# Kernel tuning notes

Measured on AMD Instinct MI355X. Metric: run time of the kernel, lower is better.

The kernel has to match this reference:

```python
import jax, jax.numpy as jnp
import numpy as np

D_MODEL = 1024
N_HEADS = 16
D_K = D_MODEL // N_HEADS  # 64, also d_v
B, S = 8, 1024


def setup_inputs() -> dict:
    key = jax.random.key(0)
    ks = jax.random.split(key, 12)
    sc = 1.0 / np.sqrt(D_MODEL)
    inp = {
        "q": jax.random.normal(ks[0], (B, S, D_MODEL), jnp.float32),
        "k": jax.random.normal(ks[1], (B, S, D_MODEL), jnp.float32),
        "v": jax.random.normal(ks[2], (B, S, D_MODEL), jnp.float32),
        # per-head projection weights stacked over heads; torch Linear stores [out,in]
        "Wq": jax.random.normal(ks[3], (N_HEADS, D_K, D_MODEL), jnp.float32) * sc,
        "bq": jax.random.normal(ks[4], (N_HEADS, D_K), jnp.float32) * sc,
        "Wk": jax.random.normal(ks[5], (N_HEADS, D_K, D_MODEL), jnp.float32) * sc,
        "bk": jax.random.normal(ks[6], (N_HEADS, D_K), jnp.float32) * sc,
        "Wv": jax.random.normal(ks[7], (N_HEADS, D_K, D_MODEL), jnp.float32) * sc,
        "bv": jax.random.normal(ks[8], (N_HEADS, D_K), jnp.float32) * sc,
        "Wf": jax.random.normal(ks[9], (D_MODEL, D_MODEL), jnp.float32) * sc,
        "bf": jax.random.normal(ks[10], (D_MODEL,), jnp.float32) * sc,
    }
    return inp


def reference(q, k, v, Wq, bq, Wk, bk, Wv, bv, Wf, bf):
    temper = jnp.asarray(D_K ** 0.5, q.dtype)
    # per-head linear projections, all heads at once: [b,s,h,dk]
    qh = jnp.einsum('bsd,hkd->bhsk', q, Wq) + bq[None, :, None, :]
    kh = jnp.einsum('bsd,hkd->bhsk', k, Wk) + bk[None, :, None, :]
    vh = jnp.einsum('bsd,hkd->bhsk', v, Wv) + bv[None, :, None, :]
    # scaled dot-product scores [b,h,s,s]
    scores = jnp.einsum('bhik,bhjk->bhij', qh, kh) / temper
    # faithful scalar-equality mask: positions exactly equal to mask (=0) -> -inf
    scores = jnp.where(scores == 0.0, -jnp.inf, scores)
    attn = jax.nn.softmax(scores, axis=-1)
    out = jnp.einsum('bhij,bhjv->bhiv', attn, vh)  # [b,h,s,dv]
    # concat heads (head order matches torch.cat over ModuleList)
    out = out.transpose(0, 2, 1, 3).reshape(out.shape[0], out.shape[2], -1)  # [b,s,d_model]
    return out @ Wf.T + bf
```

## Files before the change

### kernel.cpp

```cpp
#include <hip/hip_runtime.h>
#include <hip/hip_bf16.h>


#define D_MODEL_ 1024
#define NH_ 16
#define DK_ 64
#define B_ 8
#define S_ 1024
#define M_ (B_ * S_)

typedef __hip_bfloat16 bf16;
typedef __attribute__((ext_vector_type(8))) short short8;
typedef __attribute__((ext_vector_type(4))) short short4_t;
typedef __attribute__((ext_vector_type(4))) float f32x4;

typedef const __attribute__((address_space(1))) unsigned int* gas_u32p;
typedef __attribute__((address_space(3))) unsigned int* las_u32p;

__device__ __forceinline__ short f2bs(float x) {
  bf16 h = __float2bfloat16(x);
  return *reinterpret_cast<short*>(&h);
}

__global__ __launch_bounds__(256)
void conv_w4(const float* __restrict__ w0, const float* __restrict__ w1,
             const float* __restrict__ w2, const float* __restrict__ w3,
             bf16* __restrict__ out) {
  const float* src = (blockIdx.z == 0) ? w0 : (blockIdx.z == 1) ? w1
                   : (blockIdx.z == 2) ? w2 : w3;
  size_t i = ((size_t)blockIdx.x * 256 + threadIdx.x) * 8;
  f32x4 a = *(const f32x4*)(src + i);
  f32x4 b = *(const f32x4*)(src + i + 4);
  short8 s;
  s[0] = f2bs(a[0]); s[1] = f2bs(a[1]); s[2] = f2bs(a[2]); s[3] = f2bs(a[3]);
  s[4] = f2bs(b[0]); s[5] = f2bs(b[1]); s[6] = f2bs(b[2]); s[7] = f2bs(b[3]);
  *(short8*)((short*)out + (size_t)blockIdx.z * 1024 * 1024 + i) = s;
}

template<int BN, int AF32>
__device__ __forceinline__ void gemm_body(const void* __restrict__ A,
                                          const bf16* __restrict__ Wb,
                                          const float* __restrict__ bias,
                                          void* __restrict__ C,
                                          int cMode, float cscale, int m0, int n0)
{
  __shared__ short As[2][128 * 32];
  __shared__ short Bs[2][BN * 32];
  const int tid = threadIdx.x;
  const int lane = tid & 63;
  const int w = tid >> 6;
  const int l15 = lane & 15, quad = lane >> 4;
  const int wm = (w >> 1) * 64, wn = (w & 1) * (BN / 2);
  const int srow = lane >> 2;
  const int sslot = ((lane & 3) ^ ((lane >> 3) & 3)) * 8;
  const int rsl = (quad ^ ((l15 >> 1) & 3)) * 8;

  f32x4 au[4], av[4];
  auto loadAf = [&](int k0) {
    const float* Af = (const float*)A;
#pragma unroll
    for (int p = 0; p < 4; ++p) {
      int c = p * 256 + tid;
      int r = c >> 3, kc = (c & 7) * 8;
      const float* g = Af + (size_t)(m0 + r) * 1024 + k0 + kc;
      au[p] = *(const f32x4*)g;
      av[p] = *(const f32x4*)(g + 4);
    }
  };
  auto writeAf = [&]() {
#pragma unroll
    for (int p = 0; p < 4; ++p) {
      int c = p * 256 + tid;
      int r = c >> 3, kc = (c & 7) * 8;
      int s = (c & 3) ^ ((r >> 1) & 3);
      short8 sv;
      sv[0] = f2bs(au[p][0]); sv[1] = f2bs(au[p][1]); sv[2] = f2bs(au[p][2]); sv[3] = f2bs(au[p][3]);
      sv[4] = f2bs(av[p][0]); sv[5] = f2bs(av[p][1]); sv[6] = f2bs(av[p][2]); sv[7] = f2bs(av[p][3]);
      *(short8*)&As[kc >> 5][r * 32 + s * 8] = sv;
    }
  };

  f32x4 acc[4][BN / 32];
#pragma unroll
  for (int i = 0; i < 4; ++i)
#pragma unroll
    for (int j = 0; j < BN / 32; ++j)
      acc[i][j] = (f32x4){0.f, 0.f, 0.f, 0.f};

  if (AF32) loadAf(0);

  for (int k0 = 0; k0 < 1024; k0 += 64) {
    __syncthreads();
    if (AF32) {
      writeAf();
    } else {
      const bf16* Ab = (const bf16*)A;
#pragma unroll
      for (int sub = 0; sub < 2; ++sub)
#pragma unroll
        for (int p = 0; p < 2; ++p) {
          int r = 32 * w + 16 * p + srow;
          __builtin_amdgcn_global_load_lds(
              (gas_u32p)(const void*)(Ab + (size_t)(m0 + r) * 1024 + k0 + sub * 32 + sslot),
              (las_u32p)(void*)((char*)&As[sub][0] + w * 2048 + p * 1024), 16, 0, 0);
        }
    }
#pragma unroll
    for (int sub = 0; sub < 2; ++sub)
#pragma unroll
      for (int p = 0; p < BN / 64; ++p) {
        int r = (BN / 4) * w + 16 * p + srow;
        __builtin_amdgcn_global_load_lds(
            (gas_u32p)(const void*)(Wb + (size_t)(n0 + r) * 1024 + k0 + sub * 32 + sslot),
            (las_u32p)(void*)((char*)&Bs[sub][0] + w * (BN / 4) * 64 + p * 1024), 16, 0, 0);
      }
    __syncthreads();

    if (AF32 && k0 + 64 < 1024) loadAf(k0 + 64);

#pragma unroll
    for (int kk = 0; kk < 2; ++kk) {
      short8 af[4], bfv[BN / 32];
#pragma unroll
      for (int t = 0; t < 4; ++t)
        af[t]  = *(short8*)&As[kk][(wm + t * 16 + l15) * 32 + rsl];
#pragma unroll
      for (int t = 0; t < BN / 32; ++t)
        bfv[t] = *(short8*)&Bs[kk][(wn + t * 16 + l15) * 32 + rsl];
#pragma unroll
      for (int mt = 0; mt < 4; ++mt)
#pragma unroll
        for (int nt = 0; nt < BN / 32; ++nt)
          acc[mt][nt] = __builtin_amdgcn_mfma_f32_16x16x32_bf16(af[mt], bfv[nt], acc[mt][nt], 0, 0, 0);
    }
  }

  if (cMode == 2) {
    bf16* vt = (bf16*)C;
    const int bidx = m0 >> 10;
    const int sbase = (m0 & 1023) + wm;
#pragma unroll
    for (int nt = 0; nt < BN / 32; ++nt) {
      int n = n0 + wn + nt * 16 + l15;
      float bv = bias[n];
#pragma unroll
      for (int mt = 0; mt < 4; ++mt) {
        int s = sbase + mt * 16 + quad * 4;
        short4_t pk;
#pragma unroll
        for (int r = 0; r < 4; ++r) pk[r] = f2bs((acc[mt][nt][r] + bv) * cscale);
        *(short4_t*)((short*)vt + ((size_t)bidx * 1024 + n) * 1024 + s) = pk;
      }
    }
  } else {
#pragma unroll
    for (int nt = 0; nt < BN / 32; ++nt) {
      int col = n0 + wn + nt * 16 + l15;
      float bv = bias[col];
#pragma unroll
      for (int mt = 0; mt < 4; ++mt)
#pragma unroll
        for (int r = 0; r < 4; ++r) {
          int row = m0 + wm + mt * 16 + quad * 4 + r;
          float val = (acc[mt][nt][r] + bv) * cscale;
          if (cMode == 1) ((float*)C)[(size_t)row * 1024 + col] = val;
          else ((bf16*)C)[(size_t)row * 1024 + col] = __float2bfloat16(val);
        }
    }
  }
}

__global__ __launch_bounds__(256)
void gemm_proj(const float* __restrict__ q, const float* __restrict__ k,
               const float* __restrict__ v, const bf16* __restrict__ wq,
               const bf16* __restrict__ wk, const bf16* __restrict__ wv,
               const float* __restrict__ bq, const float* __restrict__ bk,
               const float* __restrict__ bv, void* __restrict__ cq,
               void* __restrict__ ck, void* __restrict__ cv)
{
  const int z = blockIdx.z;
  const float* A = (z == 0) ? q : (z == 1) ? k : v;
  const bf16* W  = (z == 0) ? wq : (z == 1) ? wk : wv;
  const float* bb = (z == 0) ? bq : (z == 1) ? bk : bv;
  void* C = (z == 0) ? cq : (z == 1) ? ck : cv;
  int cMode = (z == 2) ? 2 : 0;
  float cscale = (z == 0) ? 0.125f : 1.0f;
  gemm_body<128, 1>(A, W, bb, C, cMode, cscale, blockIdx.x * 128, blockIdx.y * 128);
}

__global__ __launch_bounds__(256)
void gemm_final(const bf16* __restrict__ A, const bf16* __restrict__ W,
                const float* __restrict__ bias, void* __restrict__ C)
{
  gemm_body<64, 0>(A, W, bias, C, 1, 1.0f, blockIdx.x * 128, blockIdx.y * 64);
}

__global__ __launch_bounds__(256)
void attn_mfma(const bf16* __restrict__ QH, const bf16* __restrict__ KH,
               const bf16* __restrict__ VT, bf16* __restrict__ AO)
{
  __shared__ short Ks[2][64 * 32];
  __shared__ short Vs[2][64 * 32];
  __shared__ short Ps[4][16 * 72];
  const int tid = threadIdx.x;
  const int lane = tid & 63;
  const int w = tid >> 6;
  const int l15 = lane & 15, quad = lane >> 4;
  const int q0 = blockIdx.x * 64;
  const int h = blockIdx.y, b = blockIdx.z;
  const size_t base = ((size_t)b * S_) * D_MODEL_ + (size_t)h * DK_;
  const size_t vtb  = (((size_t)b * NH_ + h) * DK_) * (size_t)S_;
  const float NEG = -1e30f;
  short* myPs = Ps[w];

  const int srow = 16 * w + (lane >> 2);
  const int sslot = ((lane & 3) ^ ((lane >> 3) & 3)) * 8;
  const int rsl = (quad ^ ((l15 >> 1) & 3)) * 8;

  short8 qa[2];
#pragma unroll
  for (int ks = 0; ks < 2; ++ks)
    qa[ks] = *(const short8*)((const short*)QH + base + (size_t)(q0 + w * 16 + l15) * D_MODEL_ + ks * 32 + quad * 8);

  float mi = NEG, li = 0.f;
  f32x4 oacc[4];
#pragma unroll
  for (int nt = 0; nt < 4; ++nt) oacc[nt] = (f32x4){0.f, 0.f, 0.f, 0.f};

  for (int j0 = 0; j0 < S_; j0 += 64) {
    __syncthreads();
#pragma unroll
    for (int sub = 0; sub < 2; ++sub) {
      __builtin_amdgcn_global_load_lds(
          (gas_u32p)(const void*)((const short*)KH + base + (size_t)(j0 + srow) * D_MODEL_ + sub * 32 + sslot),
          (las_u32p)(void*)((char*)&Ks[sub][0] + w * 1024), 16, 0, 0);
      __builtin_amdgcn_global_load_lds(
          (gas_u32p)(const void*)((const short*)VT + vtb + (size_t)srow * S_ + j0 + sub * 32 + sslot),
          (las_u32p)(void*)((char*)&Vs[sub][0] + w * 1024), 16, 0, 0);
    }
    __syncthreads();

    short8 kb[4][2], vb[4][2];
#pragma unroll
    for (int nt = 0; nt < 4; ++nt)
#pragma unroll
      for (int ks = 0; ks < 2; ++ks) {
        kb[nt][ks] = *(short8*)&Ks[ks][(nt * 16 + l15) * 32 + rsl];
        vb[nt][ks] = *(short8*)&Vs[ks][(nt * 16 + l15) * 32 + rsl];
      }

    f32x4 sacc[4];
#pragma unroll
    for (int nt = 0; nt < 4; ++nt) sacc[nt] = (f32x4){0.f, 0.f, 0.f, 0.f};
    __builtin_amdgcn_s_setprio(1);
#pragma unroll
    for (int nt = 0; nt < 4; ++nt)
#pragma unroll
      for (int ks = 0; ks < 2; ++ks)
        sacc[nt] = __builtin_amdgcn_mfma_f32_16x16x32_bf16(kb[nt][ks], qa[ks], sacc[nt], 0, 0, 0);
    __builtin_amdgcn_s_setprio(0);

    float p[4][4];
#pragma unroll
    for (int nt = 0; nt < 4; ++nt)
#pragma unroll
      for (int r = 0; r < 4; ++r) {
        float x = sacc[nt][r];
        if (x == 0.0f) x = NEG;
        p[nt][r] = x;
      }
    float mm[4];
#pragma unroll
    for (int nt = 0; nt < 4; ++nt)
      mm[nt] = fmaxf(fmaxf(p[nt][0], p[nt][1]), fmaxf(p[nt][2], p[nt][3]));
    float rm = fmaxf(fmaxf(mm[0], mm[1]), fmaxf(mm[2], mm[3]));
    rm = fmaxf(rm, __shfl_xor(rm, 16, 64));
    rm = fmaxf(rm, __shfl_xor(rm, 32, 64));

    const bool skip = __all(rm <= mi + 8.0f);
    const float nm = skip ? mi : fmaxf(mi, rm);

    float psum[4];
#pragma unroll
    for (int nt = 0; nt < 4; ++nt) {
      float e0 = __expf(p[nt][0] - nm), e1 = __expf(p[nt][1] - nm);
      float e2 = __expf(p[nt][2] - nm), e3 = __expf(p[nt][3] - nm);
      p[nt][0] = e0; p[nt][1] = e1; p[nt][2] = e2; p[nt][3] = e3;
      psum[nt] = (e0 + e1) + (e2 + e3);
    }
    float ps = (psum[0] + psum[1]) + (psum[2] + psum[3]);
    ps += __shfl_xor(ps, 16, 64);
    ps += __shfl_xor(ps, 32, 64);

    if (skip) {
      li += ps;
    } else {
      float alpha = __expf(mi - nm);
      li = li * alpha + ps;
      float ar[4];
#pragma unroll
      for (int r = 0; r < 4; ++r) ar[r] = __shfl(alpha, quad * 4 + r, 64);
#pragma unroll
      for (int nt = 0; nt < 4; ++nt)
#pragma unroll
        for (int r = 0; r < 4; ++r) oacc[nt][r] *= ar[r];
    }
    mi = nm;

#pragma unroll
    for (int nt = 0; nt < 4; ++nt) {
      short4_t pk;
#pragma unroll
      for (int r = 0; r < 4; ++r) pk[r] = f2bs(p[nt][r]);
      *(short4_t*)&myPs[l15 * 72 + nt * 16 + quad * 4] = pk;
    }

    __threadfence_block();

    short8 pa[2];
#pragma unroll
    for (int ks = 0; ks < 2; ++ks)
      pa[ks] = *(short8*)&myPs[l15 * 72 + ks * 32 + quad * 8];
    __builtin_amdgcn_s_setprio(1);
#pragma unroll
    for (int nt = 0; nt < 4; ++nt)
#pragma unroll
      for (int ks = 0; ks < 2; ++ks)
        oacc[nt] = __builtin_amdgcn_mfma_f32_16x16x32_bf16(pa[ks], vb[nt][ks], oacc[nt], 0, 0, 0);
    __builtin_amdgcn_s_setprio(0);
  }

  float lr[4];
#pragma unroll
  for (int r = 0; r < 4; ++r) lr[r] = __shfl(li, quad * 4 + r, 64);
#pragma unroll
  for (int r = 0; r < 4; ++r) {
    float inv = (lr[r] > 0.f) ? 1.0f / lr[r] : 0.f;
    int q = q0 + w * 16 + quad * 4 + r;
#pragma unroll
    for (int nt = 0; nt < 4; ++nt)
      AO[base + (size_t)q * D_MODEL_ + nt * 16 + l15] = __float2bfloat16(oacc[nt][r] * inv);
  }
}

extern "C" void kernel_launch(void* const* d_in, const int* in_sizes, int n_in,
                              void* d_out, int out_size, void* d_ws, size_t ws_size,
                              hipStream_t stream) {
  (void)in_sizes; (void)n_in; (void)out_size;
  const float* q  = (const float*)d_in[0];
  const float* k  = (const float*)d_in[1];
  const float* v  = (const float*)d_in[2];
  const float* Wq = (const float*)d_in[3];
  const float* bq = (const float*)d_in[4];
  const float* Wk = (const float*)d_in[5];
  const float* bk = (const float*)d_in[6];
  const float* Wv = (const float*)d_in[7];
  const float* bv = (const float*)d_in[8];
  const float* Wf = (const float*)d_in[9];
  const float* bF = (const float*)d_in[10];

  const size_t MB = (size_t)1024 * 1024;
  char* ws = (char*)d_ws;
  bf16* wqb = (bf16*)(ws);
  bf16* wkb = (bf16*)(ws + 2 * MB);
  bf16* wvb = (bf16*)(ws + 4 * MB);
  bf16* wfb = (bf16*)(ws + 6 * MB);
  bf16* vt  = (bf16*)(ws + 8 * MB);
  bf16* qh  = (bf16*)d_out;
  bf16* kh  = (bf16*)((char*)d_out + 16 * MB);

  const bool bigws = ws_size >= (size_t)40 * MB;
  bf16* aob = bigws ? (bf16*)(ws + 24 * MB) : qh;
  bf16* fin = bigws ? aob : (bf16*)(ws + 8 * MB);

  dim3 blk(256);

  conv_w4<<<dim3(512, 1, 4), blk, 0, stream>>>(Wq, Wk, Wv, Wf, wqb);

  gemm_proj<<<dim3(M_ / 128, D_MODEL_ / 128, 3), blk, 0, stream>>>(
      q, k, v, wqb, wkb, wvb, bq, bk, bv, qh, kh, vt);

  attn_mfma<<<dim3(S_ / 64, NH_, B_), blk, 0, stream>>>(qh, kh, vt, aob);

  if (!bigws)
    hipMemcpyAsync(ws + 8 * MB, d_out, 16 * MB, hipMemcpyDeviceToDevice, stream);

  gemm_final<<<dim3(M_ / 128, D_MODEL_ / 64), blk, 0, stream>>>(fin, wfb, bF, d_out);
}
```

Before: 330.3 us.

## Double-buffer LDS tiles in GEMM and attention to overlap loads with MFMA

Adds a second LDS buffer for the weight and activation tiles in the projection and final GEMMs, and for the K/V tiles in the attention kernel. The next tile's global-to-LDS loads are issued before computing on the current tile, and one barrier per iteration replaces the previous two. The aim is to hide global memory latency behind the MFMA work. In exchange, LDS use per block roughly doubles, which may lower occupancy, and the fp32 A path still needs an extra barrier for its register-staged write.

```diff
diff --git a/kernel.cpp b/kernel.cpp
--- a/kernel.cpp
+++ b/kernel.cpp
@@ -44,8 +44,8 @@
                                           void* __restrict__ C,
                                           int cMode, float cscale, int m0, int n0)
 {
-  __shared__ short As[2][128 * 32];
-  __shared__ short Bs[2][BN * 32];
+  __shared__ short As[(AF32 ? 1 : 2)][2][128 * 32];
+  __shared__ short Bs[2][2][BN * 32];
   const int tid = threadIdx.x;
   const int lane = tid & 63;
   const int w = tid >> 6;
@@ -76,35 +76,22 @@
       short8 sv;
       sv[0] = f2bs(au[p][0]); sv[1] = f2bs(au[p][1]); sv[2] = f2bs(au[p][2]); sv[3] = f2bs(au[p][3]);
       sv[4] = f2bs(av[p][0]); sv[5] = f2bs(av[p][1]); sv[6] = f2bs(av[p][2]); sv[7] = f2bs(av[p][3]);
-      *(short8*)&As[kc >> 5][r * 32 + s * 8] = sv;
+      *(short8*)&As[0][kc >> 5][r * 32 + s * 8] = sv;
     }
   };
-
-  f32x4 acc[4][BN / 32];
-#pragma unroll
-  for (int i = 0; i < 4; ++i)
-#pragma unroll
-    for (int j = 0; j < BN / 32; ++j)
-      acc[i][j] = (f32x4){0.f, 0.f, 0.f, 0.f};
-
-  if (AF32) loadAf(0);
-
-  for (int k0 = 0; k0 < 1024; k0 += 64) {
-    __syncthreads();
-    if (AF32) {
-      writeAf();
-    } else {
-      const bf16* Ab = (const bf16*)A;
-#pragma unroll
-      for (int sub = 0; sub < 2; ++sub)
-#pragma unroll
-        for (int p = 0; p < 2; ++p) {
-          int r = 32 * w + 16 * p + srow;
-          __builtin_amdgcn_global_load_lds(
-              (gas_u32p)(const void*)(Ab + (size_t)(m0 + r) * 1024 + k0 + sub * 32 + sslot),
-              (las_u32p)(void*)((char*)&As[sub][0] + w * 2048 + p * 1024), 16, 0, 0);
-        }
-    }
+  auto stageA = [&](int buf, int k0) {
+    const bf16* Ab = (const bf16*)A;
+#pragma unroll
+    for (int sub = 0; sub < 2; ++sub)
+#pragma unroll
+      for (int p = 0; p < 2; ++p) {
+        int r = 32 * w + 16 * p + srow;
+        __builtin_amdgcn_global_load_lds(
+            (gas_u32p)(const void*)(Ab + (size_t)(m0 + r) * 1024 + k0 + sub * 32 + sslot),
+            (las_u32p)(void*)((char*)&As[buf][sub][0] + w * 2048 + p * 1024), 16, 0, 0);
+      }
+  };
+  auto stageB = [&](int buf, int k0) {
 #pragma unroll
     for (int sub = 0; sub < 2; ++sub)
 #pragma unroll
@@ -112,26 +99,55 @@
         int r = (BN / 4) * w + 16 * p + srow;
         __builtin_amdgcn_global_load_lds(
             (gas_u32p)(const void*)(Wb + (size_t)(n0 + r) * 1024 + k0 + sub * 32 + sslot),
-            (las_u32p)(void*)((char*)&Bs[sub][0] + w * (BN / 4) * 64 + p * 1024), 16, 0, 0);
+            (las_u32p)(void*)((char*)&Bs[buf][sub][0] + w * (BN / 4) * 64 + p * 1024), 16, 0, 0);
       }
-    __syncthreads();
-
-    if (AF32 && k0 + 64 < 1024) loadAf(k0 + 64);
-
+  };
+
+  f32x4 acc[4][BN / 32];
+#pragma unroll
+  for (int i = 0; i < 4; ++i)
+#pragma unroll
+    for (int j = 0; j < BN / 32; ++j)
+      acc[i][j] = (f32x4){0.f, 0.f, 0.f, 0.f};
+
+  if (AF32) { loadAf(0); writeAf(); }
+  else      stageA(0, 0);
+  stageB(0, 0);
+  __syncthreads();
+
+  for (int k0 = 0; k0 < 1024; k0 += 64) {
+    const int cur = (k0 >> 6) & 1;
+    const int nxt = cur ^ 1;
+    const bool pf = (k0 + 64) < 1024;
+
+    if (pf) {
+      stageB(nxt, k0 + 64);
+      if (AF32) loadAf(k0 + 64);
+      else      stageA(nxt, k0 + 64);
+    }
+
+    const int ab = AF32 ? 0 : cur;
 #pragma unroll
     for (int kk = 0; kk < 2; ++kk) {
       short8 af[4], bfv[BN / 32];
 #pragma unroll
       for (int t = 0; t < 4; ++t)
-        af[t]  = *(short8*)&As[kk][(wm + t * 16 + l15) * 32 + rsl];
+        af[t]  = *(short8*)&As[ab][kk][(wm + t * 16 + l15) * 32 + rsl];
 #pragma unroll
       for (int t = 0; t < BN / 32; ++t)
-        bfv[t] = *(short8*)&Bs[kk][(wn + t * 16 + l15) * 32 + rsl];
+        bfv[t] = *(short8*)&Bs[cur][kk][(wn + t * 16 + l15) * 32 + rsl];
 #pragma unroll
       for (int mt = 0; mt < 4; ++mt)
 #pragma unroll
         for (int nt = 0; nt < BN / 32; ++nt)
           acc[mt][nt] = __builtin_amdgcn_mfma_f32_16x16x32_bf16(af[mt], bfv[nt], acc[mt][nt], 0, 0, 0);
+    }
+
+    __syncthreads();
+
+    if (AF32 && pf) {
+      writeAf();
+      __syncthreads();
     }
   }
 
@@ -199,8 +215,8 @@
 void attn_mfma(const bf16* __restrict__ QH, const bf16* __restrict__ KH,
                const bf16* __restrict__ VT, bf16* __restrict__ AO)
 {
-  __shared__ short Ks[2][64 * 32];
-  __shared__ short Vs[2][64 * 32];
+  __shared__ short Ks[2][2][64 * 32];
+  __shared__ short Vs[2][2][64 * 32];
   __shared__ short Ps[4][16 * 72];
   const int tid = threadIdx.x;
   const int lane = tid & 63;
@@ -217,36 +233,43 @@
   const int sslot = ((lane & 3) ^ ((lane >> 3) & 3)) * 8;
   const int rsl = (quad ^ ((l15 >> 1) & 3)) * 8;
 
-  short8 qa[2];
-#pragma unroll
-  for (int ks = 0; ks < 2; ++ks)
-    qa[ks] = *(const short8*)((const short*)QH + base + (size_t)(q0 + w * 16 + l15) * D_MODEL_ + ks * 32 + quad * 8);
-
-  float mi = NEG, li = 0.f;
-  f32x4 oacc[4];
-#pragma unroll
-  for (int nt = 0; nt < 4; ++nt) oacc[nt] = (f32x4){0.f, 0.f, 0.f, 0.f};
-
-  for (int j0 = 0; j0 < S_; j0 += 64) {
-    __syncthreads();
+  auto stage = [&](int buf, int j0) {
 #pragma unroll
     for (int sub = 0; sub < 2; ++sub) {
       __builtin_amdgcn_global_load_lds(
           (gas_u32p)(const void*)((const short*)KH + base + (size_t)(j0 + srow) * D_MODEL_ + sub * 32 + sslot),
-          (las_u32p)(void*)((char*)&Ks[sub][0] + w * 1024), 16, 0, 0);
+          (las_u32p)(void*)((char*)&Ks[buf][sub][0] + w * 1024), 16, 0, 0);
       __builtin_amdgcn_global_load_lds(
           (gas_u32p)(const void*)((const short*)VT + vtb + (size_t)srow * S_ + j0 + sub * 32 + sslot),
-          (las_u32p)(void*)((char*)&Vs[sub][0] + w * 1024), 16, 0, 0);
-    }
-    __syncthreads();
+          (las_u32p)(void*)((char*)&Vs[buf][sub][0] + w * 1024), 16, 0, 0);
+    }
+  };
+
+  short8 qa[2];
+#pragma unroll
+  for (int ks = 0; ks < 2; ++ks)
+    qa[ks] = *(const short8*)((const short*)QH + base + (size_t)(q0 + w * 16 + l15) * D_MODEL_ + ks * 32 + quad * 8);
+
+  float mi = NEG, li = 0.f;
+  f32x4 oacc[4];
+#pragma unroll
+  for (int nt = 0; nt < 4; ++nt) oacc[nt] = (f32x4){0.f, 0.f, 0.f, 0.f};
+
+  stage(0, 0);
+  __syncthreads();
+
+  for (int j0 = 0; j0 < S_; j0 += 64) {
+    const int cur = (j0 >> 6) & 1;
+    const int nxt = cur ^ 1;
+    if (j0 + 64 < S_) stage(nxt, j0 + 64);
 
     short8 kb[4][2], vb[4][2];
 #pragma unroll
     for (int nt = 0; nt < 4; ++nt)
 #pragma unroll
       for (int ks = 0; ks < 2; ++ks) {
-        kb[nt][ks] = *(short8*)&Ks[ks][(nt * 16 + l15) * 32 + rsl];
-        vb[nt][ks] = *(short8*)&Vs[ks][(nt * 16 + l15) * 32 + rsl];
+        kb[nt][ks] = *(short8*)&Ks[cur][ks][(nt * 16 + l15) * 32 + rsl];
+        vb[nt][ks] = *(short8*)&Vs[cur][ks][(nt * 16 + l15) * 32 + rsl];
       }
 
     f32x4 sacc[4];
@@ -328,6 +351,8 @@
       for (int ks = 0; ks < 2; ++ks)
         oacc[nt] = __builtin_amdgcn_mfma_f32_16x16x32_bf16(pa[ks], vb[nt][ks], oacc[nt], 0, 0, 0);
     __builtin_amdgcn_s_setprio(0);
+
+    __syncthreads();
   }
 
   float lr[4];
```

New measurement: 363.7 us. 1.1x slower.

## Remap block indices to XCD-local tiles and switch softmax to exp2

Applied to the files above, without the earlier changes.

All three kernels now take a flat 1-D grid and remap each block so that consecutive blocks on the same XCD (block index mod 8) work on neighbouring M tiles or the same batch/head. This is meant to raise L2 reuse of the A rows, weights and K/V within each XCD's private L2. The Q projection scale now folds in log2(e), so the attention softmax can use exp2f instead of __expf, with the rescale-skip threshold scaled to match. If the math is consistent this saves a multiply per exponential, but it depends on the folded scale and the zero-equality mask staying correct.

```diff
diff --git a/kernel.cpp b/kernel.cpp
--- a/kernel.cpp
+++ b/kernel.cpp
@@ -178,21 +178,35 @@
                const float* __restrict__ bv, void* __restrict__ cq,
                void* __restrict__ ck, void* __restrict__ cv)
 {
-  const int z = blockIdx.z;
+  const int f = blockIdx.x;
+  const int xcd = f & 7;
+  const int i = f >> 3;
+  const int xp = i / 24;
+  const int yz = i - xp * 24;
+  const int z = yz >> 3;
+  const int y = yz & 7;
+  const int x = xcd * 8 + xp;
+
   const float* A = (z == 0) ? q : (z == 1) ? k : v;
   const bf16* W  = (z == 0) ? wq : (z == 1) ? wk : wv;
   const float* bb = (z == 0) ? bq : (z == 1) ? bk : bv;
   void* C = (z == 0) ? cq : (z == 1) ? ck : cv;
   int cMode = (z == 2) ? 2 : 0;
-  float cscale = (z == 0) ? 0.125f : 1.0f;
-  gemm_body<128, 1>(A, W, bb, C, cMode, cscale, blockIdx.x * 128, blockIdx.y * 128);
+  float cscale = (z == 0) ? 0.18033688011112042f : 1.0f;
+  gemm_body<128, 1>(A, W, bb, C, cMode, cscale, x * 128, y * 128);
 }
 
 __global__ __launch_bounds__(256)
 void gemm_final(const bf16* __restrict__ A, const bf16* __restrict__ W,
                 const float* __restrict__ bias, void* __restrict__ C)
 {
-  gemm_body<64, 0>(A, W, bias, C, 1, 1.0f, blockIdx.x * 128, blockIdx.y * 64);
+  const int f = blockIdx.x;
+  const int xcd = f & 7;
+  const int i = f >> 3;
+  const int xp = i >> 4;
+  const int y = i & 15;
+  const int x = xcd * 8 + xp;
+  gemm_body<64, 0>(A, W, bias, C, 1, 1.0f, x * 128, y * 64);
 }
 
 __global__ __launch_bounds__(256)
@@ -206,11 +220,20 @@
   const int lane = tid & 63;
   const int w = tid >> 6;
   const int l15 = lane & 15, quad = lane >> 4;
-  const int q0 = blockIdx.x * 64;
-  const int h = blockIdx.y, b = blockIdx.z;
+
+  const int f = blockIdx.x;
+  const int xcd = f & 7;
+  const int i = f >> 3;
+  const int qt = i & 15;
+  const int bhl = i >> 4;
+  const int bh = xcd * 16 + bhl;
+  const int b = bh >> 4, h = bh & 15;
+  const int q0 = qt * 64;
+
   const size_t base = ((size_t)b * S_) * D_MODEL_ + (size_t)h * DK_;
   const size_t vtb  = (((size_t)b * NH_ + h) * DK_) * (size_t)S_;
   const float NEG = -1e30f;
+  const float THR = 11.54156032f;
   short* myPs = Ps[w];
 
   const int srow = 16 * w + (lane >> 2);
@@ -277,14 +300,14 @@
     rm = fmaxf(rm, __shfl_xor(rm, 16, 64));
     rm = fmaxf(rm, __shfl_xor(rm, 32, 64));
 
-    const bool skip = __all(rm <= mi + 8.0f);
+    const bool skip = __all(rm <= mi + THR);
     const float nm = skip ? mi : fmaxf(mi, rm);
 
     float psum[4];
 #pragma unroll
     for (int nt = 0; nt < 4; ++nt) {
-      float e0 = __expf(p[nt][0] - nm), e1 = __expf(p[nt][1] - nm);
-      float e2 = __expf(p[nt][2] - nm), e3 = __expf(p[nt][3] - nm);
+      float e0 = exp2f(p[nt][0] - nm), e1 = exp2f(p[nt][1] - nm);
+      float e2 = exp2f(p[nt][2] - nm), e3 = exp2f(p[nt][3] - nm);
       p[nt][0] = e0; p[nt][1] = e1; p[nt][2] = e2; p[nt][3] = e3;
       psum[nt] = (e0 + e1) + (e2 + e3);
     }
@@ -295,7 +318,7 @@
     if (skip) {
       li += ps;
     } else {
-      float alpha = __expf(mi - nm);
+      float alpha = exp2f(mi - nm);
       li = li * alpha + ps;
       float ar[4];
 #pragma unroll
@@ -377,13 +400,13 @@
 
   conv_w4<<<dim3(512, 1, 4), blk, 0, stream>>>(Wq, Wk, Wv, Wf, wqb);
 
-  gemm_proj<<<dim3(M_ / 128, D_MODEL_ / 128, 3), blk, 0, stream>>>(
+  gemm_proj<<<dim3(1536), blk, 0, stream>>>(
       q, k, v, wqb, wkb, wvb, bq, bk, bv, qh, kh, vt);
 
-  attn_mfma<<<dim3(S_ / 64, NH_, B_), blk, 0, stream>>>(qh, kh, vt, aob);
+  attn_mfma<<<dim3(2048), blk, 0, stream>>>(qh, kh, vt, aob);
 
   if (!bigws)
     hipMemcpyAsync(ws + 8 * MB, d_out, 16 * MB, hipMemcpyDeviceToDevice, stream);
 
-  gemm_final<<<dim3(M_ / 128, D_MODEL_ / 64), blk, 0, stream>>>(fin, wfb, bF, d_out);
-}
+  gemm_final<<<dim3(1024), blk, 0, stream>>>(fin, wfb, bF, d_out);
+}
```

Result: slower. 350.4 us (+6.1%).

## Process two query tiles per wave in attention and use exp2 softmax

Applied to the files above, without the earlier changes.

Each attention block now covers 128 queries, two 16-row groups per wave, so every K/V tile loaded into shared memory is reused twice and the block count halves. Separately, the Q projection scale now includes log2(e), so the softmax can use exp2f instead of __expf, and the lazy-rescale threshold is adjusted to match. The cost is more registers per thread (two accumulator sets) and fewer blocks, which may lower occupancy and parallelism.

```diff
diff --git a/kernel.cpp b/kernel.cpp
--- a/kernel.cpp
+++ b/kernel.cpp
@@ -184,7 +184,7 @@
   const float* bb = (z == 0) ? bq : (z == 1) ? bk : bv;
   void* C = (z == 0) ? cq : (z == 1) ? ck : cv;
   int cMode = (z == 2) ? 2 : 0;
-  float cscale = (z == 0) ? 0.125f : 1.0f;
+  float cscale = (z == 0) ? 0.18033688011112042f : 1.0f;
   gemm_body<128, 1>(A, W, bb, C, cMode, cscale, blockIdx.x * 128, blockIdx.y * 128);
 }
 
@@ -201,31 +201,36 @@
 {
   __shared__ short Ks[2][64 * 32];
   __shared__ short Vs[2][64 * 32];
-  __shared__ short Ps[4][16 * 72];
+  __shared__ short Ps[4][2][16 * 72];
   const int tid = threadIdx.x;
   const int lane = tid & 63;
   const int w = tid >> 6;
   const int l15 = lane & 15, quad = lane >> 4;
-  const int q0 = blockIdx.x * 64;
+  const int q0 = blockIdx.x * 128;
   const int h = blockIdx.y, b = blockIdx.z;
   const size_t base = ((size_t)b * S_) * D_MODEL_ + (size_t)h * DK_;
   const size_t vtb  = (((size_t)b * NH_ + h) * DK_) * (size_t)S_;
   const float NEG = -1e30f;
-  short* myPs = Ps[w];
+  const float THR = 11.54156032f;
 
   const int srow = 16 * w + (lane >> 2);
   const int sslot = ((lane & 3) ^ ((lane >> 3) & 3)) * 8;
   const int rsl = (quad ^ ((l15 >> 1) & 3)) * 8;
 
-  short8 qa[2];
-#pragma unroll
-  for (int ks = 0; ks < 2; ++ks)
-    qa[ks] = *(const short8*)((const short*)QH + base + (size_t)(q0 + w * 16 + l15) * D_MODEL_ + ks * 32 + quad * 8);
-
-  float mi = NEG, li = 0.f;
-  f32x4 oacc[4];
-#pragma unroll
-  for (int nt = 0; nt < 4; ++nt) oacc[nt] = (f32x4){0.f, 0.f, 0.f, 0.f};
+  short8 qa[2][2];
+#pragma unroll
+  for (int g = 0; g < 2; ++g)
+#pragma unroll
+    for (int ks = 0; ks < 2; ++ks)
+      qa[g][ks] = *(const short8*)((const short*)QH + base
+                   + (size_t)(q0 + w * 32 + g * 16 + l15) * D_MODEL_ + ks * 32 + quad * 8);
+
+  float mi[2] = {NEG, NEG}, li[2] = {0.f, 0.f};
+  f32x4 oacc[2][4];
+#pragma unroll
+  for (int g = 0; g < 2; ++g)
+#pragma unroll
+    for (int nt = 0; nt < 4; ++nt) oacc[g][nt] = (f32x4){0.f, 0.f, 0.f, 0.f};
 
   for (int j0 = 0; j0 < S_; j0 += 64) {
     __syncthreads();
@@ -249,97 +254,104 @@
         vb[nt][ks] = *(short8*)&Vs[ks][(nt * 16 + l15) * 32 + rsl];
       }
 
-    f32x4 sacc[4];
-#pragma unroll
-    for (int nt = 0; nt < 4; ++nt) sacc[nt] = (f32x4){0.f, 0.f, 0.f, 0.f};
-    __builtin_amdgcn_s_setprio(1);
-#pragma unroll
-    for (int nt = 0; nt < 4; ++nt)
+#pragma unroll
+    for (int g = 0; g < 2; ++g) {
+      f32x4 sacc[4];
+#pragma unroll
+      for (int nt = 0; nt < 4; ++nt) sacc[nt] = (f32x4){0.f, 0.f, 0.f, 0.f};
+      __builtin_amdgcn_s_setprio(1);
+#pragma unroll
+      for (int nt = 0; nt < 4; ++nt)
+#pragma unroll
+        for (int ks = 0; ks < 2; ++ks)
+          sacc[nt] = __builtin_amdgcn_mfma_f32_16x16x32_bf16(kb[nt][ks], qa[g][ks], sacc[nt], 0, 0, 0);
+      __builtin_amdgcn_s_setprio(0);
+
+      float p[4][4];
+#pragma unroll
+      for (int nt = 0; nt < 4; ++nt)
+#pragma unroll
+        for (int r = 0; r < 4; ++r) {
+          float x = sacc[nt][r];
+          if (x == 0.0f) x = NEG;
+          p[nt][r] = x;
+        }
+      float mm[4];
+#pragma unroll
+      for (int nt = 0; nt < 4; ++nt)
+        mm[nt] = fmaxf(fmaxf(p[nt][0], p[nt][1]), fmaxf(p[nt][2], p[nt][3]));
+      float rm = fmaxf(fmaxf(mm[0], mm[1]), fmaxf(mm[2], mm[3]));
+      rm = fmaxf(rm, __shfl_xor(rm, 16, 64));
+      rm = fmaxf(rm, __shfl_xor(rm, 32, 64));
+
+      const bool skip = __all(rm <= mi[g] + THR);
+      const float nm = skip ? mi[g] : fmaxf(mi[g], rm);
+
+      float psum[4];
+#pragma unroll
+      for (int nt = 0; nt < 4; ++nt) {
+        float e0 = exp2f(p[nt][0] - nm), e1 = exp2f(p[nt][1] - nm);
+        float e2 = exp2f(p[nt][2] - nm), e3 = exp2f(p[nt][3] - nm);
+        p[nt][0] = e0; p[nt][1] = e1; p[nt][2] = e2; p[nt][3] = e3;
+        psum[nt] = (e0 + e1) + (e2 + e3);
+      }
+      float ps = (psum[0] + psum[1]) + (psum[2] + psum[3]);
+      ps += __shfl_xor(ps, 16, 64);
+      ps += __shfl_xor(ps, 32, 64);
+
+      if (skip) {
+        li[g] += ps;
+      } else {
+        float alpha = exp2f(mi[g] - nm);
+        li[g] = li[g] * alpha + ps;
+        float ar[4];
+#pragma unroll
+        for (int r = 0; r < 4; ++r) ar[r] = __shfl(alpha, quad * 4 + r, 64);
+#pragma unroll
+        for (int nt = 0; nt < 4; ++nt)
+#pragma unroll
+          for (int r = 0; r < 4; ++r) oacc[g][nt][r] *= ar[r];
+      }
+      mi[g] = nm;
+
+      short* myPs = Ps[w][g];
+#pragma unroll
+      for (int nt = 0; nt < 4; ++nt) {
+        short4_t pk;
+#pragma unroll
+        for (int r = 0; r < 4; ++r) pk[r] = f2bs(p[nt][r]);
+        *(short4_t*)&myPs[l15 * 72 + nt * 16 + quad * 4] = pk;
+      }
+
+      __threadfence_block();
+
+      short8 pa[2];
 #pragma unroll
       for (int ks = 0; ks < 2; ++ks)
-        sacc[nt] = __builtin_amdgcn_mfma_f32_16x16x32_bf16(kb[nt][ks], qa[ks], sacc[nt], 0, 0, 0);
-    __builtin_amdgcn_s_setprio(0);
-
-    float p[4][4];
-#pragma unroll
-    for (int nt = 0; nt < 4; ++nt)
-#pragma unroll
-      for (int r = 0; r < 4; ++r) {
-        float x = sacc[nt][r];
-        if (x == 0.0f) x = NEG;
-        p[nt][r] = x;
-      }
-    float mm[4];
-#pragma unroll
-    for (int nt = 0; nt < 4; ++nt)
-      mm[nt] = fmaxf(fmaxf(p[nt][0], p[nt][1]), fmaxf(p[nt][2], p[nt][3]));
-    float rm = fmaxf(fmaxf(mm[0], mm[1]), fmaxf(mm[2], mm[3]));
-    rm = fmaxf(rm, __shfl_xor(rm, 16, 64));
-    rm = fmaxf(rm, __shfl_xor(rm, 32, 64));
-
-    const bool skip = __all(rm <= mi + 8.0f);
-    const float nm = skip ? mi : fmaxf(mi, rm);
-
-    float psum[4];
-#pragma unroll
-    for (int nt = 0; nt < 4; ++nt) {
-      float e0 = __expf(p[nt][0] - nm), e1 = __expf(p[nt][1] - nm);
-      float e2 = __expf(p[nt][2] - nm), e3 = __expf(p[nt][3] - nm);
-      p[nt][0] = e0; p[nt][1] = e1; p[nt][2] = e2; p[nt][3] = e3;
-      psum[nt] = (e0 + e1) + (e2 + e3);
-    }
-    float ps = (psum[0] + psum[1]) + (psum[2] + psum[3]);
-    ps += __shfl_xor(ps, 16, 64);
-    ps += __shfl_xor(ps, 32, 64);
-
-    if (skip) {
-      li += ps;
-    } else {
-      float alpha = __expf(mi - nm);
-      li = li * alpha + ps;
-      float ar[4];
-#pragma unroll
-      for (int r = 0; r < 4; ++r) ar[r] = __shfl(alpha, quad * 4 + r, 64);
+        pa[ks] = *(short8*)&myPs[l15 * 72 + ks * 32 + quad * 8];
+      __builtin_amdgcn_s_setprio(1);
 #pragma unroll
       for (int nt = 0; nt < 4; ++nt)
 #pragma unroll
-        for (int r = 0; r < 4; ++r) oacc[nt][r] *= ar[r];
-    }
-    mi = nm;
-
-#pragma unroll
-    for (int nt = 0; nt < 4; ++nt) {
-      short4_t pk;
-#pragma unroll
-      for (int r = 0; r < 4; ++r) pk[r] = f2bs(p[nt][r]);
-      *(short4_t*)&myPs[l15 * 72 + nt * 16 + quad * 4] = pk;
-    }
-
-    __threadfence_block();
-
-    short8 pa[2];
-#pragma unroll
-    for (int ks = 0; ks < 2; ++ks)
-      pa[ks] = *(short8*)&myPs[l15 * 72 + ks * 32 + quad * 8];
-    __builtin_amdgcn_s_setprio(1);
-#pragma unroll
-    for (int nt = 0; nt < 4; ++nt)
-#pragma unroll
-      for (int ks = 0; ks < 2; ++ks)
-        oacc[nt] = __builtin_amdgcn_mfma_f32_16x16x32_bf16(pa[ks], vb[nt][ks], oacc[nt], 0, 0, 0);
-    __builtin_amdgcn_s_setprio(0);
+        for (int ks = 0; ks < 2; ++ks)
+          oacc[g][nt] = __builtin_amdgcn_mfma_f32_16x16x32_bf16(pa[ks], vb[nt][ks], oacc[g][nt], 0, 0, 0);
+      __builtin_amdgcn_s_setprio(0);
+    }
   }
 
-  float lr[4];
-#pragma unroll
-  for (int r = 0; r < 4; ++r) lr[r] = __shfl(li, quad * 4 + r, 64);
-#pragma unroll
-  for (int r = 0; r < 4; ++r) {
-    float inv = (lr[r] > 0.f) ? 1.0f / lr[r] : 0.f;
-    int q = q0 + w * 16 + quad * 4 + r;
-#pragma unroll
-    for (int nt = 0; nt < 4; ++nt)
-      AO[base + (size_t)q * D_MODEL_ + nt * 16 + l15] = __float2bfloat16(oacc[nt][r] * inv);
+#pragma unroll
+  for (int g = 0; g < 2; ++g) {
+    float lr[4];
+#pragma unroll
+    for (int r = 0; r < 4; ++r) lr[r] = __shfl(li[g], quad * 4 + r, 64);
+#pragma unroll
+    for (int r = 0; r < 4; ++r) {
+      float inv = (lr[r] > 0.f) ? 1.0f / lr[r] : 0.f;
+      int qq = q0 + w * 32 + g * 16 + quad * 4 + r;
+#pragma unroll
+      for (int nt = 0; nt < 4; ++nt)
+        AO[base + (size_t)qq * D_MODEL_ + nt * 16 + l15] = __float2bfloat16(oacc[g][nt][r] * inv);
+    }
   }
 }
 
@@ -380,7 +392,7 @@
   gemm_proj<<<dim3(M_ / 128, D_MODEL_ / 128, 3), blk, 0, stream>>>(
       q, k, v, wqb, wkb, wvb, bq, bk, bv, qh, kh, vt);
 
-  attn_mfma<<<dim3(S_ / 64, NH_, B_), blk, 0, stream>>>(qh, kh, vt, aob);
+  attn_mfma<<<dim3(S_ / 128, NH_, B_), blk, 0, stream>>>(qh, kh, vt, aob);
 
   if (!bigws)
     hipMemcpyAsync(ws + 8 * MB, d_out, 16 * MB, hipMemcpyDeviceToDevice, stream);
```

Result: slower. 347.2 us (+5.1%).
